# Kernel optimization log

Measured on AMD Instinct MI355X. Metric: run time of the kernel, lower is better.

## Reference

```python
import jax, jax.numpy as jnp
import numpy as np
import math

WS = 7          # window side
NH = 4          # num heads
CIN = 128       # in_channels
HD = CIN // NH  # head dim
SCALE = 1.0 / math.sqrt(HD)


def _rel_index():
    # standard Swin relative-position index, [WS*WS, WS*WS]
    c = np.stack(np.meshgrid(np.arange(WS), np.arange(WS), indexing='ij'), 0).reshape(2, -1)
    r = (c[:, :, None] - c[:, None, :]).transpose(1, 2, 0)  # [n, n, 2]
    r[..., 0] += WS - 1
    r[..., 1] += WS - 1
    r[..., 0] *= 2 * WS - 1
    return r.sum(-1)


def setup_inputs() -> dict:
    key = jax.random.key(0)
    ks = jax.random.split(key, 12)
    B, C, H, W = 64, CIN, 56, 56
    s = 0.02
    return {
        'query': jax.random.normal(ks[0], (B, C, H, W), jnp.float32),
        'key': jax.random.normal(ks[1], (B, C, H, W), jnp.float32),
        'value': jax.random.normal(ks[2], (B, C, H, W), jnp.float32),
        'Wq': jax.random.normal(ks[3], (C, C), jnp.float32) * s,
        'bq': jnp.zeros((C,), jnp.float32),
        'Wk': jax.random.normal(ks[4], (C, C), jnp.float32) * s,
        'bk': jnp.zeros((C,), jnp.float32),
        'Wv': jax.random.normal(ks[5], (C, C), jnp.float32) * s,
        'bv': jnp.zeros((C,), jnp.float32),
        'Wo': jax.random.normal(ks[6], (C, C), jnp.float32) * s,
        'bo': jnp.zeros((C,), jnp.float32),
        'rpb_table': jax.random.normal(ks[7], ((2 * WS - 1) ** 2, NH), jnp.float32) * s,
    }


def reference(query, key, value, Wq, bq, Wk, bk, Wv, bv, Wo, bo, rpb_table):
    B, C, H, W = query.shape
    nh, nw = H // WS, W // WS
    n = WS * WS

    def to_seq(x):
        # [B, C, H, W] -> [(B*nh*nw), n, C] window partition
        x = x.reshape(B, C, nh, WS, nw, WS)
        return x.transpose(0, 2, 4, 3, 5, 1).reshape(B * nh * nw, n, C)

    def to_spatial(x):
        x = x.reshape(B, nh, nw, WS, WS, C)
        return x.transpose(0, 5, 1, 3, 2, 4).reshape(B, C, H, W)

    q = to_seq(query) @ Wq.T + bq
    k = to_seq(key) @ Wk.T + bk
    v = to_seq(value) @ Wv.T + bv

    def heads(x):
        return x.reshape(-1, n, NH, HD).transpose(0, 2, 1, 3)  # [b, h, n, d]

    q, k, v = heads(q), heads(k), heads(v)

    score = jnp.einsum('bhid,bhjd->bhij', q, k) * SCALE
    idx = _rel_index()  # static numpy [n, n]
    bias = rpb_table[idx.reshape(-1)].reshape(n, n, NH).transpose(2, 0, 1)  # [h, n, n]
    score = score + bias[None]
    ctx = jax.nn.softmax(score, axis=-1)
    out = jnp.einsum('bhij,bhjd->bhid', ctx, v)
    out = out.transpose(0, 2, 1, 3).reshape(-1, n, C)
    x = out @ Wo.T + bo
    return to_spatial(x), ctx
```

## Files before the change

kernel.cpp:

```cpp
#include <hip/hip_runtime.h>

#define NTOK 49
#define CC   128
#define NHEADS 4
#define HWW  56
#define HW2  3136
#define SCALE_F 0.17677669529663687f

typedef __attribute__((ext_vector_type(8))) short s16x8;
typedef __attribute__((ext_vector_type(4))) float f32x4;
typedef __attribute__((ext_vector_type(16))) float f32x16;

static __device__ __forceinline__ unsigned short f2bf(float f) {
  unsigned int u = __float_as_uint(f);
  u += 0x7fffu + ((u >> 16) & 1u);
  return (unsigned short)(u >> 16);
}
static __device__ __forceinline__ float bf2f(unsigned short h) {
  return __uint_as_float(((unsigned int)h) << 16);
}
static __device__ __forceinline__ unsigned int pkbf(float lo, float hi) {
  return (unsigned int)f2bf(lo) | ((unsigned int)f2bf(hi) << 16);
}
static __device__ __forceinline__ int swz4(int row, int col) { return col ^ ((row & 3) << 3); }

union FragU { s16x8 v; unsigned int u[4]; };

__global__ void wconv_kernel(const float* __restrict__ Wq, const float* __restrict__ Wk,
                             const float* __restrict__ Wv, const float* __restrict__ Wo,
                             unsigned short* __restrict__ dst) {
  int i = blockIdx.x * 256 + threadIdx.x;
  const float* src = (i < 16384) ? Wq : (i < 32768) ? Wk : (i < 49152) ? Wv : Wo;
  float v = src[i & 16383];
  if (i < 16384) v *= SCALE_F;
  dst[i] = f2bf(v);
}

__global__ __launch_bounds__(256, 3)
void winattn_kernel(const float* __restrict__ Xq, const float* __restrict__ Xk,
                    const float* __restrict__ Xv,
                    const unsigned short* __restrict__ Wbf,
                    const float* __restrict__ bq, const float* __restrict__ bk,
                    const float* __restrict__ bv, const float* __restrict__ bo,
                    const float* __restrict__ rpb,
                    float* __restrict__ out_x,
                    float* __restrict__ out_ctx)
{
  __shared__ alignas(16) unsigned short smem[25984];
  unsigned short* Buf0 = smem;
  unsigned short* Buf1 = smem + 6272;
  unsigned short* VT   = smem + 12544;
  unsigned short* Buf2 = smem + 19712;

  const int tid = threadIdx.x;
  const int wv  = tid >> 6;
  const int l   = tid & 63;
  const int lr  = l & 15;
  const int lg  = l >> 4;
  const int c31 = l & 31;
  const int hi  = l >> 5;

  const int win  = (blockIdx.x & 7) * 512 + (blockIdx.x >> 3);
  const int bimg = win >> 6;
  const int r0   = ((win >> 3) & 7) * 7;
  const int c0   = (win & 7) * 7;

  {
    unsigned int* vz = (unsigned int*)VT;
    #pragma unroll
    for (int i = 0; i < 14; ++i) vz[tid + i*256] = 0u;
    int s = tid & 63, g = tid >> 6;
    if (s < NTOK) {
      int si = s / 7, sj = s - si*7;
      size_t base = (size_t)bimg*CC*HW2 + (size_t)(r0+si)*HWW + (c0+sj);
      int rb = s * CC;
      #pragma unroll 8
      for (int cc = 0; cc < 32; ++cc) {
        int ci = g*32 + cc;
        size_t off = base + (size_t)ci * HW2;
        int di = rb + swz4(s, ci);
        Buf0[di] = f2bf(Xq[off]);
        Buf1[di] = f2bf(Xk[off]);
        Buf2[di] = f2bf(Xv[off]);
      }
    }
  }
  __syncthreads();

  auto projR = [&](const unsigned short* __restrict__ src, const unsigned short* __restrict__ Wg,
                   const float* __restrict__ bias, float bscale,
                   f32x4 (&acc)[4][2], float (&bb)[2]) {
    s16x8 bfr[2][4];
    #pragma unroll
    for (int ntl = 0; ntl < 2; ++ntl) {
      int col = wv*32 + ntl*16 + lr;
      bb[ntl] = bias[col] * bscale;
      #pragma unroll
      for (int ks = 0; ks < 4; ++ks)
        bfr[ntl][ks] = *(const s16x8*)(Wg + col*CC + ks*32 + lg*8);
    }
    #pragma unroll
    for (int mt = 0; mt < 4; ++mt) {
      int ar = mt*16 + lr;
      s16x8 af[4];
      #pragma unroll
      for (int ks = 0; ks < 4; ++ks)
        af[ks] = *(const s16x8*)(src + ar*CC + swz4(ar, ks*32 + lg*8));
      #pragma unroll
      for (int ntl = 0; ntl < 2; ++ntl) {
        f32x4 a = {0.f,0.f,0.f,0.f};
        #pragma unroll
        for (int ks = 0; ks < 4; ++ks)
          a = __builtin_amdgcn_mfma_f32_16x16x32_bf16(af[ks], bfr[ntl][ks], a, 0,0,0);
        acc[mt][ntl] = a;
      }
    }
  };
  auto projW = [&](unsigned short* __restrict__ dst, f32x4 (&acc)[4][2], float (&bb)[2]) {
    #pragma unroll
    for (int mt = 0; mt < 4; ++mt) {
      #pragma unroll
      for (int ntl = 0; ntl < 2; ++ntl) {
        int col = wv*32 + ntl*16 + lr;
        #pragma unroll
        for (int r = 0; r < 4; ++r) {
          int row = mt*16 + lg*4 + r;
          if (row < NTOK)
            dst[row*CC + swz4(row, col)] = f2bf(acc[mt][ntl][r] + bb[ntl]);
        }
      }
    }
  };

  f32x4 acc[4][2]; float bb[2];
  projR(Buf0, Wbf, bq, SCALE_F, acc, bb);
  __syncthreads();
  projW(Buf0, acc, bb);
  projR(Buf1, Wbf + 16384, bk, 1.f, acc, bb);
  __syncthreads();
  projW(Buf1, acc, bb);
  {
    s16x8 bfr[2][4]; float vb[2];
    #pragma unroll
    for (int ntl = 0; ntl < 2; ++ntl) {
      int col = wv*32 + ntl*16 + lr;
      vb[ntl] = bv[col];
      #pragma unroll
      for (int ks = 0; ks < 4; ++ks)
        bfr[ntl][ks] = *(const s16x8*)(Wbf + 32768 + col*CC + ks*32 + lg*8);
    }
    #pragma unroll
    for (int mt = 0; mt < 4; ++mt) {
      int ar = mt*16 + lr;
      s16x8 af[4];
      #pragma unroll
      for (int ks = 0; ks < 4; ++ks)
        af[ks] = *(const s16x8*)(Buf2 + ar*CC + swz4(ar, ks*32 + lg*8));
      #pragma unroll
      for (int ntl = 0; ntl < 2; ++ntl) {
        f32x4 a = {0.f,0.f,0.f,0.f};
        #pragma unroll
        for (int ks = 0; ks < 4; ++ks)
          a = __builtin_amdgcn_mfma_f32_16x16x32_bf16(af[ks], bfr[ntl][ks], a, 0,0,0);
        int col = wv*32 + ntl*16 + lr;
        #pragma unroll
        for (int r = 0; r < 4; ++r) {
          int row = mt*16 + lg*4 + r;
          if (row < NTOK) VT[col*56 + row] = f2bf(a[r] + vb[ntl]);
        }
      }
    }
  }
  __syncthreads();

  {
    const int h = wv;
    s16x8 ak[2][2], av[4];
    #pragma unroll
    for (int kt = 0; kt < 2; ++kt) {
      int krow = kt*32 + c31; if (krow > 48) krow = 48;
      #pragma unroll
      for (int ks = 0; ks < 2; ++ks)
        ak[kt][ks] = *(const s16x8*)(Buf1 + krow*CC + swz4(krow, h*32 + ks*16 + hi*8));
    }
    #pragma unroll
    for (int kk = 0; kk < 4; ++kk)
      av[kk] = *(const s16x8*)(VT + (h*32 + c31)*56 + kk*16 + hi*8);
    size_t cbase = ((size_t)win*NHEADS + h)*(NTOK*NTOK);
    unsigned short* PL = Buf2 + h*1568;

    #pragma unroll
    for (int qh = 0; qh < 2; ++qh) {
      int q = qh*32 + c31;
      int qrow = q > 48 ? 48 : q;
      s16x8 bqf[2];
      #pragma unroll
      for (int ks = 0; ks < 2; ++ks)
        bqf[ks] = *(const s16x8*)(Buf0 + qrow*CC + swz4(qrow, h*32 + ks*16 + hi*8));
      f32x16 s0 = {0,0,0,0,0,0,0,0,0,0,0,0,0,0,0,0};
      f32x16 s1 = {0,0,0,0,0,0,0,0,0,0,0,0,0,0,0,0};
      s0 = __builtin_amdgcn_mfma_f32_32x32x16_bf16(ak[0][0], bqf[0], s0, 0,0,0);
      s0 = __builtin_amdgcn_mfma_f32_32x32x16_bf16(ak[0][1], bqf[1], s0, 0,0,0);
      s1 = __builtin_amdgcn_mfma_f32_32x32x16_bf16(ak[1][0], bqf[0], s1, 0,0,0);
      s1 = __builtin_amdgcn_mfma_f32_32x32x16_bf16(ak[1][1], bqf[1], s1, 0,0,0);
      int i1 = q / 7, j1 = q - (q/7)*7;
      float mx = -1e30f;
      #pragma unroll
      for (int r = 0; r < 16; ++r) {
        int kb = (r&3) + 8*(r>>2) + 4*hi;
        { int ktok = kb;
          float s = -1e30f;
          if (q < NTOK && ktok < NTOK) {
            int i2 = ktok/7, j2 = ktok - (ktok/7)*7;
            s = s0[r] + rpb[((i1-i2+6)*13 + (j1-j2+6))*NHEADS + h];
          }
          s0[r] = s; mx = fmaxf(mx, s); }
        { int ktok = kb + 32;
          float s = -1e30f;
          if (q < NTOK && ktok < NTOK) {
            int i2 = ktok/7, j2 = ktok - (ktok/7)*7;
            s = s1[r] + rpb[((i1-i2+6)*13 + (j1-j2+6))*NHEADS + h];
          }
          s1[r] = s; mx = fmaxf(mx, s); }
      }
      mx = fmaxf(mx, __shfl_xor(mx, 32));
      float sum = 0.f;
      #pragma unroll
      for (int r = 0; r < 16; ++r) { s0[r] = __expf(s0[r]-mx); sum += s0[r]; }
      #pragma unroll
      for (int r = 0; r < 16; ++r) { s1[r] = __expf(s1[r]-mx); sum += s1[r]; }
      sum += __shfl_xor(sum, 32);
      float rinv = 1.f / sum;
      #pragma unroll
      for (int r = 0; r < 16; ++r) { s0[r] *= rinv; s1[r] *= rinv; }
      if (q < NTOK) {
        #pragma unroll
        for (int r = 0; r < 16; ++r) {
          int kb = (r&3) + 8*(r>>2) + 4*hi;
          PL[c31*NTOK + kb] = f2bf(s0[r]);
          if (kb + 32 < NTOK) PL[c31*NTOK + kb + 32] = f2bf(s1[r]);
        }
      }
      f32x16 pacc = {0,0,0,0,0,0,0,0,0,0,0,0,0,0,0,0};
      auto pvstep = [&](f32x16& e, const s16x8& a0, const s16x8& a1) {
        unsigned int w0m0 = pkbf(e[0],e[1]),   w0m1 = pkbf(e[2],e[3]);
        unsigned int w1m0 = pkbf(e[4],e[5]),   w1m1 = pkbf(e[6],e[7]);
        unsigned int w2m0 = pkbf(e[8],e[9]),   w2m1 = pkbf(e[10],e[11]);
        unsigned int w3m0 = pkbf(e[12],e[13]), w3m1 = pkbf(e[14],e[15]);
        unsigned int p0m0 = __shfl_xor((int)w0m0,32), p0m1 = __shfl_xor((int)w0m1,32);
        unsigned int p1m0 = __shfl_xor((int)w1m0,32), p1m1 = __shfl_xor((int)w1m1,32);
        unsigned int p2m0 = __shfl_xor((int)w2m0,32), p2m1 = __shfl_xor((int)w2m1,32);
        unsigned int p3m0 = __shfl_xor((int)w3m0,32), p3m1 = __shfl_xor((int)w3m1,32);
        FragU f;
        f.u[0] = hi ? p1m0 : w0m0;  f.u[1] = hi ? p1m1 : w0m1;
        f.u[2] = hi ? w1m0 : p0m0;  f.u[3] = hi ? w1m1 : p0m1;
        pacc = __builtin_amdgcn_mfma_f32_32x32x16_bf16(a0, f.v, pacc, 0,0,0);
        f.u[0] = hi ? p3m0 : w2m0;  f.u[1] = hi ? p3m1 : w2m1;
        f.u[2] = hi ? w3m0 : p2m0;  f.u[3] = hi ? w3m1 : p2m1;
        pacc = __builtin_amdgcn_mfma_f32_32x32x16_bf16(a1, f.v, pacc, 0,0,0);
      };
      pvstep(s0, av[0], av[1]);
      pvstep(s1, av[2], av[3]);
      {
        const int cnt = (qh == 0) ? 32*NTOK : (NTOK-32)*NTOK;
        size_t gb = cbase + (size_t)qh*32*NTOK;
        #pragma unroll
        for (int base = 0; base < cnt; base += 64) {
          int idx = base + l;
          if (idx < cnt) out_ctx[gb + idx] = bf2f(PL[idx]);
        }
      }
      if (q < NTOK) {
        #pragma unroll
        for (int r = 0; r < 16; ++r) {
          int d = (r&3) + 8*(r>>2) + 4*hi;
          Buf0[q*CC + swz4(q, h*32 + d)] = f2bf(pacc[r]);
        }
      }
    }
  }
  __syncthreads();

  {
    const unsigned short* Wg = Wbf + 49152;
    s16x8 bfr[2][4]; float ob[2];
    #pragma unroll
    for (int ntl = 0; ntl < 2; ++ntl) {
      int col = wv*32 + ntl*16 + lr;
      ob[ntl] = bo[col];
      #pragma unroll
      for (int ks = 0; ks < 4; ++ks)
        bfr[ntl][ks] = *(const s16x8*)(Wg + col*CC + ks*32 + lg*8);
    }
    #pragma unroll
    for (int mt = 0; mt < 4; ++mt) {
      int ar = mt*16 + lr;
      s16x8 af[4];
      #pragma unroll
      for (int ks = 0; ks < 4; ++ks)
        af[ks] = *(const s16x8*)(Buf0 + ar*CC + swz4(ar, ks*32 + lg*8));
      #pragma unroll
      for (int ntl = 0; ntl < 2; ++ntl) {
        f32x4 a = {0.f,0.f,0.f,0.f};
        #pragma unroll
        for (int ks = 0; ks < 4; ++ks)
          a = __builtin_amdgcn_mfma_f32_16x16x32_bf16(af[ks], bfr[ntl][ks], a, 0,0,0);
        int col = wv*32 + ntl*16 + lr;
        #pragma unroll
        for (int r = 0; r < 4; ++r) {
          int row = mt*16 + lg*4 + r;
          if (row < NTOK) {
            int ii = row / 7, jj = row - (row/7)*7;
            size_t off = ((size_t)(bimg*CC + col))*HW2 + (size_t)(r0+ii)*HWW + (c0+jj);
            out_x[off] = a[r] + ob[ntl];
          }
        }
      }
    }
  }
}

extern "C" void kernel_launch(void* const* d_in, const int* in_sizes, int n_in,
                              void* d_out, int out_size, void* d_ws, size_t ws_size,
                              hipStream_t stream) {
  (void)in_sizes; (void)n_in; (void)out_size; (void)ws_size;
  const float* query = (const float*)d_in[0];
  const float* key   = (const float*)d_in[1];
  const float* value = (const float*)d_in[2];
  const float* Wq = (const float*)d_in[3];
  const float* bq = (const float*)d_in[4];
  const float* Wk = (const float*)d_in[5];
  const float* bk = (const float*)d_in[6];
  const float* Wv = (const float*)d_in[7];
  const float* bv = (const float*)d_in[8];
  const float* Wo = (const float*)d_in[9];
  const float* bo = (const float*)d_in[10];
  const float* rpb = (const float*)d_in[11];

  unsigned short* Wbf = (unsigned short*)d_ws;
  float* out_x   = (float*)d_out;
  float* out_ctx = out_x + (size_t)64*CC*HW2;

  wconv_kernel<<<256, 256, 0, stream>>>(Wq, Wk, Wv, Wo, Wbf);
  winattn_kernel<<<4096, 256, 0, stream>>>(query, key, value, Wbf, bq, bk, bv, bo, rpb,
                                           out_x, out_ctx);
}
```

Baseline: 314.1 us.

## Precompute expanded relative bias, pack input staging, stage output through LDS

A prep kernel now expands the relative-position bias table into a dense per-head [k][q] array, which replaces per-element index arithmetic and gathers inside the softmax loop. The input staging loop loads four channels per iteration and writes packed 8-byte bf16 stores. The LDS swizzle widens from 4-row to 8-row XOR to reduce bank conflicts. The output projection is written to an LDS transpose buffer and then stored to global memory in token-contiguous order instead of with channel-strided scalar stores. In exchange, the kernel uses extra workspace memory and reuses LDS for the output buffer.

```diff
diff --git a/kernel.cpp b/kernel.cpp
--- a/kernel.cpp
+++ b/kernel.cpp
@@ -10,6 +10,7 @@
 typedef __attribute__((ext_vector_type(8))) short s16x8;
 typedef __attribute__((ext_vector_type(4))) float f32x4;
 typedef __attribute__((ext_vector_type(16))) float f32x16;
+typedef __attribute__((ext_vector_type(2))) unsigned int u32x2;
 
 static __device__ __forceinline__ unsigned short f2bf(float f) {
   unsigned int u = __float_as_uint(f);
@@ -22,27 +23,38 @@
 static __device__ __forceinline__ unsigned int pkbf(float lo, float hi) {
   return (unsigned int)f2bf(lo) | ((unsigned int)f2bf(hi) << 16);
 }
-static __device__ __forceinline__ int swz4(int row, int col) { return col ^ ((row & 3) << 3); }
+static __device__ __forceinline__ int swz8(int row, int col) { return col ^ ((row & 7) << 3); }
 
 union FragU { s16x8 v; unsigned int u[4]; };
 
-__global__ void wconv_kernel(const float* __restrict__ Wq, const float* __restrict__ Wk,
-                             const float* __restrict__ Wv, const float* __restrict__ Wo,
-                             unsigned short* __restrict__ dst) {
+__global__ void prep_kernel(const float* __restrict__ Wq, const float* __restrict__ Wk,
+                            const float* __restrict__ Wv, const float* __restrict__ Wo,
+                            const float* __restrict__ rpb,
+                            unsigned short* __restrict__ dstW, float* __restrict__ dstB) {
   int i = blockIdx.x * 256 + threadIdx.x;
-  const float* src = (i < 16384) ? Wq : (i < 32768) ? Wk : (i < 49152) ? Wv : Wo;
-  float v = src[i & 16383];
-  if (i < 16384) v *= SCALE_F;
-  dst[i] = f2bf(v);
+  if (i < 65536) {
+    const float* src = (i < 16384) ? Wq : (i < 32768) ? Wk : (i < 49152) ? Wv : Wo;
+    float v = src[i & 16383];
+    if (i < 16384) v *= SCALE_F;
+    dstW[i] = f2bf(v);
+  } else {
+    int j = i - 65536;
+    if (j < NHEADS*NTOK*NTOK) {
+      int h = j / (NTOK*NTOK), rem = j - h*(NTOK*NTOK);
+      int k = rem / NTOK, q = rem - k*NTOK;
+      int qi = q/7, qj = q - qi*7, ki = k/7, kj = k - ki*7;
+      dstB[j] = rpb[((qi-ki+6)*13 + (qj-kj+6))*NHEADS + h];
+    }
+  }
 }
 
 __global__ __launch_bounds__(256, 3)
 void winattn_kernel(const float* __restrict__ Xq, const float* __restrict__ Xk,
                     const float* __restrict__ Xv,
                     const unsigned short* __restrict__ Wbf,
+                    const float* __restrict__ Biasg,
                     const float* __restrict__ bq, const float* __restrict__ bk,
                     const float* __restrict__ bv, const float* __restrict__ bo,
-                    const float* __restrict__ rpb,
                     float* __restrict__ out_x,
                     float* __restrict__ out_ctx)
 {
@@ -51,6 +63,7 @@
   unsigned short* Buf1 = smem + 6272;
   unsigned short* VT   = smem + 12544;
   unsigned short* Buf2 = smem + 19712;
+  float* Obnc = (float*)(smem + 12544);
 
   const int tid = threadIdx.x;
   const int wv  = tid >> 6;
@@ -73,15 +86,20 @@
     if (s < NTOK) {
       int si = s / 7, sj = s - si*7;
       size_t base = (size_t)bimg*CC*HW2 + (size_t)(r0+si)*HWW + (c0+sj);
-      int rb = s * CC;
-      #pragma unroll 8
-      for (int cc = 0; cc < 32; ++cc) {
-        int ci = g*32 + cc;
+      #pragma unroll 4
+      for (int cp = 0; cp < 8; ++cp) {
+        int ci = g*32 + cp*4;
         size_t off = base + (size_t)ci * HW2;
-        int di = rb + swz4(s, ci);
-        Buf0[di] = f2bf(Xq[off]);
-        Buf1[di] = f2bf(Xk[off]);
-        Buf2[di] = f2bf(Xv[off]);
+        float q0 = Xq[off], q1 = Xq[off+HW2], q2 = Xq[off+2*HW2], q3 = Xq[off+3*HW2];
+        float k0 = Xk[off], k1 = Xk[off+HW2], k2 = Xk[off+2*HW2], k3 = Xk[off+3*HW2];
+        float v0 = Xv[off], v1 = Xv[off+HW2], v2 = Xv[off+2*HW2], v3 = Xv[off+3*HW2];
+        int di = s*CC + swz8(s, ci);
+        u32x2 pq = {pkbf(q0,q1), pkbf(q2,q3)};
+        u32x2 pk = {pkbf(k0,k1), pkbf(k2,k3)};
+        u32x2 pv = {pkbf(v0,v1), pkbf(v2,v3)};
+        *(u32x2*)(Buf0 + di) = pq;
+        *(u32x2*)(Buf1 + di) = pk;
+        *(u32x2*)(Buf2 + di) = pv;
       }
     }
   }
@@ -105,7 +123,7 @@
       s16x8 af[4];
       #pragma unroll
       for (int ks = 0; ks < 4; ++ks)
-        af[ks] = *(const s16x8*)(src + ar*CC + swz4(ar, ks*32 + lg*8));
+        af[ks] = *(const s16x8*)(src + ar*CC + swz8(ar, ks*32 + lg*8));
       #pragma unroll
       for (int ntl = 0; ntl < 2; ++ntl) {
         f32x4 a = {0.f,0.f,0.f,0.f};
@@ -126,7 +144,7 @@
         for (int r = 0; r < 4; ++r) {
           int row = mt*16 + lg*4 + r;
           if (row < NTOK)
-            dst[row*CC + swz4(row, col)] = f2bf(acc[mt][ntl][r] + bb[ntl]);
+            dst[row*CC + swz8(row, col)] = f2bf(acc[mt][ntl][r] + bb[ntl]);
         }
       }
     }
@@ -155,7 +173,7 @@
       s16x8 af[4];
       #pragma unroll
       for (int ks = 0; ks < 4; ++ks)
-        af[ks] = *(const s16x8*)(Buf2 + ar*CC + swz4(ar, ks*32 + lg*8));
+        af[ks] = *(const s16x8*)(Buf2 + ar*CC + swz8(ar, ks*32 + lg*8));
       #pragma unroll
       for (int ntl = 0; ntl < 2; ++ntl) {
         f32x4 a = {0.f,0.f,0.f,0.f};
@@ -175,13 +193,14 @@
 
   {
     const int h = wv;
+    const float* Bh = Biasg + h*(NTOK*NTOK);
     s16x8 ak[2][2], av[4];
     #pragma unroll
     for (int kt = 0; kt < 2; ++kt) {
       int krow = kt*32 + c31; if (krow > 48) krow = 48;
       #pragma unroll
       for (int ks = 0; ks < 2; ++ks)
-        ak[kt][ks] = *(const s16x8*)(Buf1 + krow*CC + swz4(krow, h*32 + ks*16 + hi*8));
+        ak[kt][ks] = *(const s16x8*)(Buf1 + krow*CC + swz8(krow, h*32 + ks*16 + hi*8));
     }
     #pragma unroll
     for (int kk = 0; kk < 4; ++kk)
@@ -196,32 +215,24 @@
       s16x8 bqf[2];
       #pragma unroll
       for (int ks = 0; ks < 2; ++ks)
-        bqf[ks] = *(const s16x8*)(Buf0 + qrow*CC + swz4(qrow, h*32 + ks*16 + hi*8));
+        bqf[ks] = *(const s16x8*)(Buf0 + qrow*CC + swz8(qrow, h*32 + ks*16 + hi*8));
       f32x16 s0 = {0,0,0,0,0,0,0,0,0,0,0,0,0,0,0,0};
       f32x16 s1 = {0,0,0,0,0,0,0,0,0,0,0,0,0,0,0,0};
       s0 = __builtin_amdgcn_mfma_f32_32x32x16_bf16(ak[0][0], bqf[0], s0, 0,0,0);
       s0 = __builtin_amdgcn_mfma_f32_32x32x16_bf16(ak[0][1], bqf[1], s0, 0,0,0);
       s1 = __builtin_amdgcn_mfma_f32_32x32x16_bf16(ak[1][0], bqf[0], s1, 0,0,0);
       s1 = __builtin_amdgcn_mfma_f32_32x32x16_bf16(ak[1][1], bqf[1], s1, 0,0,0);
-      int i1 = q / 7, j1 = q - (q/7)*7;
       float mx = -1e30f;
       #pragma unroll
       for (int r = 0; r < 16; ++r) {
         int kb = (r&3) + 8*(r>>2) + 4*hi;
-        { int ktok = kb;
-          float s = -1e30f;
-          if (q < NTOK && ktok < NTOK) {
-            int i2 = ktok/7, j2 = ktok - (ktok/7)*7;
-            s = s0[r] + rpb[((i1-i2+6)*13 + (j1-j2+6))*NHEADS + h];
-          }
-          s0[r] = s; mx = fmaxf(mx, s); }
-        { int ktok = kb + 32;
-          float s = -1e30f;
-          if (q < NTOK && ktok < NTOK) {
-            int i2 = ktok/7, j2 = ktok - (ktok/7)*7;
-            s = s1[r] + rpb[((i1-i2+6)*13 + (j1-j2+6))*NHEADS + h];
-          }
-          s1[r] = s; mx = fmaxf(mx, s); }
+        float v0 = -1e30f, v1 = -1e30f;
+        if (q < NTOK) {
+          v0 = s0[r] + Bh[kb*NTOK + q];
+          if (kb + 32 < NTOK) v1 = s1[r] + Bh[(kb+32)*NTOK + q];
+        }
+        s0[r] = v0; mx = fmaxf(mx, v0);
+        s1[r] = v1; mx = fmaxf(mx, v1);
       }
       mx = fmaxf(mx, __shfl_xor(mx, 32));
       float sum = 0.f;
@@ -274,7 +285,7 @@
         #pragma unroll
         for (int r = 0; r < 16; ++r) {
           int d = (r&3) + 8*(r>>2) + 4*hi;
-          Buf0[q*CC + swz4(q, h*32 + d)] = f2bf(pacc[r]);
+          Buf0[q*CC + swz8(q, h*32 + d)] = f2bf(pacc[r]);
         }
       }
     }
@@ -283,6 +294,7 @@
 
   {
     const unsigned short* Wg = Wbf + 49152;
+    float* Of = Obnc + wv*1600;
     s16x8 bfr[2][4]; float ob[2];
     #pragma unroll
     for (int ntl = 0; ntl < 2; ++ntl) {
@@ -298,23 +310,29 @@
       s16x8 af[4];
       #pragma unroll
       for (int ks = 0; ks < 4; ++ks)
-        af[ks] = *(const s16x8*)(Buf0 + ar*CC + swz4(ar, ks*32 + lg*8));
+        af[ks] = *(const s16x8*)(Buf0 + ar*CC + swz8(ar, ks*32 + lg*8));
       #pragma unroll
       for (int ntl = 0; ntl < 2; ++ntl) {
         f32x4 a = {0.f,0.f,0.f,0.f};
         #pragma unroll
         for (int ks = 0; ks < 4; ++ks)
           a = __builtin_amdgcn_mfma_f32_16x16x32_bf16(af[ks], bfr[ntl][ks], a, 0,0,0);
-        int col = wv*32 + ntl*16 + lr;
         #pragma unroll
         for (int r = 0; r < 4; ++r) {
           int row = mt*16 + lg*4 + r;
-          if (row < NTOK) {
-            int ii = row / 7, jj = row - (row/7)*7;
-            size_t off = ((size_t)(bimg*CC + col))*HW2 + (size_t)(r0+ii)*HWW + (c0+jj);
-            out_x[off] = a[r] + ob[ntl];
-          }
-        }
+          if (row < NTOK)
+            Of[(ntl*16 + lr)*50 + row] = a[r] + ob[ntl];
+        }
+      }
+    }
+    int chb = bimg*CC + wv*32;
+    #pragma unroll
+    for (int it = 0; it < 25; ++it) {
+      int e = it*64 + l;
+      if (e < 32*NTOK) {
+        int ch = e / NTOK, tok = e - ch*NTOK;
+        int si = tok / 7, sj = tok - si*7;
+        out_x[(size_t)(chb + ch)*HW2 + (size_t)(r0+si)*HWW + (c0+sj)] = Of[ch*50 + tok];
       }
     }
   }
@@ -338,10 +356,11 @@
   const float* rpb = (const float*)d_in[11];
 
   unsigned short* Wbf = (unsigned short*)d_ws;
+  float* Biasg = (float*)((char*)d_ws + 131072);
   float* out_x   = (float*)d_out;
   float* out_ctx = out_x + (size_t)64*CC*HW2;
 
-  wconv_kernel<<<256, 256, 0, stream>>>(Wq, Wk, Wv, Wo, Wbf);
-  winattn_kernel<<<4096, 256, 0, stream>>>(query, key, value, Wbf, bq, bk, bv, bo, rpb,
-                                           out_x, out_ctx);
-}
+  prep_kernel<<<294, 256, 0, stream>>>(Wq, Wk, Wv, Wo, rpb, Wbf, Biasg);
+  winattn_kernel<<<4096, 256, 0, stream>>>(query, key, value, Wbf, Biasg,
+                                           bq, bk, bv, bo, out_x, out_ctx);
+}
```

Result: faster. 264.6 us (-15.8%).
